# Kernel optimization log

Hardware: AMD Instinct MI355X
Metric: run time of the kernel (lower is better)

The kernel has to match this reference:

```python
import jax, jax.numpy as jnp
import numpy as np

H, D, DK, DV = 16, 1024, 64, 64
B, SQ, SK = 4, 1024, 1024
SCALE = float(np.power(D, 0.5))  # original scales by sqrt(num_dim), not sqrt(num_dim_k)


def setup_inputs() -> dict:
    key = jax.random.key(0)
    ks = jax.random.split(key, 8)
    xav_k = float(np.sqrt(2.0 / (D + DK)))
    xav_v = float(np.sqrt(2.0 / (D + DV)))
    return {
        "query": jax.random.normal(ks[0], (B, SQ, D), jnp.float32),
        "key": jax.random.normal(ks[1], (B, SK, D), jnp.float32),
        "value": jax.random.normal(ks[2], (B, SK, D), jnp.float32),
        "w_q": jax.random.normal(ks[3], (H, D, DK), jnp.float32) * xav_k,
        "w_k": jax.random.normal(ks[4], (H, D, DK), jnp.float32) * xav_k,
        "w_v": jax.random.normal(ks[5], (H, D, DV), jnp.float32) * xav_v,
        "w_proj": jax.random.normal(ks[6], (D, H * DV), jnp.float32) * float(np.sqrt(1.0 / (H * DV))),
        "b_proj": jnp.zeros((D,), jnp.float32),
    }


def reference(query, key, value, w_q, w_k, w_v, w_proj, b_proj):
    # per-head projections: [b,s,d] x [h,d,k] -> [b,h,s,k]
    q = jnp.einsum("bsd,hdk->bhsk", query, w_q)
    k = jnp.einsum("bsd,hdk->bhsk", key, w_k)
    v = jnp.einsum("bsd,hdv->bhsv", value, w_v)
    # scaled dot-product attention (dropout = identity in eval)
    scores = jnp.einsum("bhqk,bhsk->bhqs", q, k) / SCALE
    attn = jax.nn.softmax(scores, axis=-1)  # [b,h,sq,sk]
    out = jnp.einsum("bhqs,bhsv->bhqv", attn, v)
    # original: outs laid out [h*b, sq, dv], split by batch and cat on feature dim
    # -> heads concatenated along last dim: [b, sq, h*dv]
    out = out.transpose(0, 2, 1, 3).reshape(B, SQ, H * DV)
    out = out @ w_proj.T + b_proj  # Linear(H*DV -> D)
    # attns returned with head-major batch: [h*b, sq, sk]
    attns = attn.transpose(1, 0, 2, 3).reshape(H * B, SQ, SK)
    return (out, attns)
```

## Files before the change

### kernel.cpp

```cpp
#include <hip/hip_runtime.h>
#include <cstdint>

typedef __bf16 bf16;
typedef bf16 bf16x8 __attribute__((ext_vector_type(8)));
typedef bf16 bf16x4 __attribute__((ext_vector_type(4)));
typedef float f32x4 __attribute__((ext_vector_type(4)));

#define MFMA16(a, b, c) __builtin_amdgcn_mfma_f32_16x16x32_bf16((a), (b), (c), 0, 0, 0)

#define GLOBAL_TO_LDS16(gptr, lptr)                                          \
  __builtin_amdgcn_global_load_lds(                                          \
      (const __attribute__((address_space(1))) void*)(gptr),                 \
      (__attribute__((address_space(3))) void*)(lptr), 16, 0, 0)


__global__ __launch_bounds__(256) void cvt_all(
    const float* __restrict__ q, const float* __restrict__ k,
    const float* __restrict__ v, const float* __restrict__ wp,
    bf16* __restrict__ qb, bf16* __restrict__ kb,
    bf16* __restrict__ vb, bf16* __restrict__ wpb) {
  long i4 = ((long)blockIdx.x * 256 + threadIdx.x) * 4;
  const float* src;
  bf16* dst;
  long off;
  if (i4 < 4194304) {
    src = q; dst = qb; off = i4;
  } else if (i4 < 8388608) {
    src = k; dst = kb; off = i4 - 4194304;
  } else if (i4 < 12582912) {
    src = v; dst = vb; off = i4 - 8388608;
  } else {
    src = wp; dst = wpb; off = i4 - 12582912;
  }
  float4 f = *(const float4*)(src + off);
  bf16x4 o;
  o[0] = (bf16)f.x; o[1] = (bf16)f.y; o[2] = (bf16)f.z; o[3] = (bf16)f.w;
  *(bf16x4*)(dst + off) = o;
}

__global__ __launch_bounds__(256) void wtrans(
    const float* __restrict__ wq, const float* __restrict__ wk,
    const float* __restrict__ wv, bf16* __restrict__ wqT,
    bf16* __restrict__ wkT, bf16* __restrict__ wvT) {
  int z = blockIdx.z;
  const float* src = (z == 0) ? wq : ((z == 1) ? wk : wv);
  bf16* dst = (z == 0) ? wqT : ((z == 1) ? wkT : wvT);
  int t = blockIdx.x * 256 + threadIdx.x;
  int d = t & 1023;
  int r = t >> 10;
  int h = r >> 6, kk = r & 63;
  dst[t] = (bf16)src[(h << 16) + (d << 6) + kk];
}

__device__ __forceinline__ void gemm_mainloop(
    const bf16* __restrict__ A, const bf16* __restrict__ BT, bf16* As,
    bf16* Bs, int m0, int n0, f32x4 acc[4][4]) {
  const int tid = threadIdx.x;
  const int lane = tid & 63, wave = tid >> 6;
  const int wm = wave >> 1, wn = wave & 1;
  const int ln = lane & 15, ko8 = (lane >> 4) * 8;
  const int c0 = tid, c1 = 256 + tid;
  const int r0 = c0 >> 2, q0 = c0 & 3;
  const int r1 = c1 >> 2, q1 = c1 & 3;

  for (int k0 = 0; k0 < 1024; k0 += 32) {
    GLOBAL_TO_LDS16(A + (long)(m0 + r0) * 1024 + k0 + q0 * 8, As + c0 * 8);
    GLOBAL_TO_LDS16(A + (long)(m0 + r1) * 1024 + k0 + q1 * 8, As + c1 * 8);
    GLOBAL_TO_LDS16(BT + (long)(n0 + r0) * 1024 + k0 + q0 * 8, Bs + c0 * 8);
    GLOBAL_TO_LDS16(BT + (long)(n0 + r1) * 1024 + k0 + q1 * 8, Bs + c1 * 8);
    __syncthreads();
    bf16x8 af[4], bg[4];
#pragma unroll
    for (int t = 0; t < 4; ++t) {
      af[t] = *(const bf16x8*)(As + (wm * 64 + t * 16 + ln) * 32 + ko8);
      bg[t] = *(const bf16x8*)(Bs + (wn * 64 + t * 16 + ln) * 32 + ko8);
    }
#pragma unroll
    for (int i = 0; i < 4; ++i)
#pragma unroll
      for (int j = 0; j < 4; ++j) acc[i][j] = MFMA16(af[i], bg[j], acc[i][j]);
    __syncthreads();
  }
}

__global__ __launch_bounds__(256) void qkv_gemm(
    const bf16* __restrict__ qb, const bf16* __restrict__ kb,
    const bf16* __restrict__ vb, const bf16* __restrict__ wqT,
    const bf16* __restrict__ wkT, const bf16* __restrict__ wvT,
    bf16* __restrict__ Qd, bf16* __restrict__ Kd, bf16* __restrict__ Vtd) {
  __shared__ bf16 As[128 * 32];
  __shared__ bf16 Bs[128 * 32];
  int z = blockIdx.z;
  const bf16* A = (z == 0) ? qb : ((z == 1) ? kb : vb);
  const bf16* BT = (z == 0) ? wqT : ((z == 1) ? wkT : wvT);
  int m0 = blockIdx.x * 128, n0 = blockIdx.y * 128;
  f32x4 acc[4][4] = {};
  gemm_mainloop(A, BT, As, Bs, m0, n0, acc);

  const int tid = threadIdx.x, lane = tid & 63, wave = tid >> 6;
  const int wm = wave >> 1, wn = wave & 1, ln = lane & 15, lk = lane >> 4;
  const float alpha = (z == 0) ? 0.03125f : 1.0f;
  bf16* dstQK = (z == 0) ? Qd : Kd;
#pragma unroll
  for (int ti = 0; ti < 4; ++ti)
#pragma unroll
    for (int tj = 0; tj < 4; ++tj) {
      int n = n0 + wn * 64 + tj * 16 + ln;
#pragma unroll
      for (int i = 0; i < 4; ++i) {
        int m = m0 + wm * 64 + ti * 16 + lk * 4 + i;
        float vv = acc[ti][tj][i] * alpha;
        if (z <= 1) {
          long addr =
              ((((long)(m >> 10) * 16 + (n >> 6)) << 10) + (m & 1023)) * 64 +
              (n & 63);
          dstQK[addr] = (bf16)vv;
        } else {
          long addr =
              ((((long)(m >> 10) * 16 + (n >> 6)) << 6) + (n & 63)) * 1024 +
              (m & 1023);
          Vtd[addr] = (bf16)vv;
        }
      }
    }
}

__global__ __launch_bounds__(256) void attn_kernel(
    const bf16* __restrict__ Qd, const bf16* __restrict__ Kd,
    const bf16* __restrict__ Vtd, float* __restrict__ attns,
    bf16* __restrict__ Ob) {
  __shared__ bf16 P[16 * 1024];
  __shared__ float wstats[4][16][2];

  int qt = blockIdx.x, h = blockIdx.y, b = blockIdx.z;
  int q0 = qt * 16;
  int tid = threadIdx.x, lane = tid & 63, wave = tid >> 6;
  int ln = lane & 15, lk = lane >> 4;

  const bf16* Qbh = Qd + (((long)(b * 16 + h)) << 10) * 64;
  const bf16* Kbh = Kd + (((long)(b * 16 + h)) << 10) * 64;
  const bf16* Vbh = Vtd + (((long)(b * 16 + h)) << 6) * 1024;

  bf16x8 aq0 = *(const bf16x8*)(Qbh + (long)(q0 + ln) * 64 + lk * 8);
  bf16x8 aq1 = *(const bf16x8*)(Qbh + (long)(q0 + ln) * 64 + 32 + lk * 8);

  f32x4 sacc[16];
#pragma unroll
  for (int t = 0; t < 16; ++t) {
    int sk0 = wave * 256 + t * 16;
    f32x4 a = {0.f, 0.f, 0.f, 0.f};
    bf16x8 bk0 = *(const bf16x8*)(Kbh + (long)(sk0 + ln) * 64 + lk * 8);
    bf16x8 bk1 = *(const bf16x8*)(Kbh + (long)(sk0 + ln) * 64 + 32 + lk * 8);
    a = MFMA16(aq0, bk0, a);
    a = MFMA16(aq1, bk1, a);
    sacc[t] = a;
  }

  float mw[4], lw[4];
#pragma unroll
  for (int i = 0; i < 4; ++i) {
    float m = sacc[0][i];
#pragma unroll
    for (int t = 1; t < 16; ++t) m = fmaxf(m, sacc[t][i]);
#pragma unroll
    for (int off = 1; off < 16; off <<= 1) m = fmaxf(m, __shfl_xor(m, off, 64));
    mw[i] = m;
  }
#pragma unroll
  for (int i = 0; i < 4; ++i) {
    float s = 0.f;
#pragma unroll
    for (int t = 0; t < 16; ++t) {
      float e = __expf(sacc[t][i] - mw[i]);
      sacc[t][i] = e;
      s += e;
    }
#pragma unroll
    for (int off = 1; off < 16; off <<= 1) s += __shfl_xor(s, off, 64);
    lw[i] = s;
  }
  if (ln == 0) {
#pragma unroll
    for (int i = 0; i < 4; ++i) {
      wstats[wave][lk * 4 + i][0] = mw[i];
      wstats[wave][lk * 4 + i][1] = lw[i];
    }
  }
  __syncthreads();

  float fscale[4];
#pragma unroll
  for (int i = 0; i < 4; ++i) {
    int r = lk * 4 + i;
    float M = fmaxf(fmaxf(wstats[0][r][0], wstats[1][r][0]),
                    fmaxf(wstats[2][r][0], wstats[3][r][0]));
    float L = 0.f;
#pragma unroll
    for (int w = 0; w < 4; ++w)
      L += wstats[w][r][1] * __expf(wstats[w][r][0] - M);
    fscale[i] = __expf(mw[i] - M) / L;
  }

  float* arow_base = attns + ((((long)(h * 4 + b)) << 10) + q0) * 1024;
#pragma unroll
  for (int t = 0; t < 16; ++t) {
    int col = wave * 256 + t * 16 + ln;
    int g = col >> 3, cw = col & 7;
#pragma unroll
    for (int i = 0; i < 4; ++i) {
      int r = lk * 4 + i;
      float a = sacc[t][i] * fscale[i];
      arow_base[(long)r * 1024 + col] = a;
      P[(r << 10) + ((g ^ (r & 7)) << 3) + cw] = (bf16)a;
    }
  }
  __syncthreads();

  f32x4 oacc = {0.f, 0.f, 0.f, 0.f};
#pragma unroll 4
  for (int s0 = 0; s0 < 1024; s0 += 32) {
    int g = (s0 >> 3) + lk;
    bf16x8 ap = *(const bf16x8*)(P + (ln << 10) + ((g ^ (ln & 7)) << 3));
    bf16x8 bv =
        *(const bf16x8*)(Vbh + (long)(wave * 16 + ln) * 1024 + s0 + lk * 8);
    oacc = MFMA16(ap, bv, oacc);
  }
#pragma unroll
  for (int i = 0; i < 4; ++i) {
    int qrow = q0 + lk * 4 + i;
    Ob[((((long)b) << 10) + qrow) * 1024 + (h << 6) + wave * 16 + ln] =
        (bf16)oacc[i];
  }
}

__global__ __launch_bounds__(256) void out_gemm(
    const bf16* __restrict__ Ob, const bf16* __restrict__ wpb,
    const float* __restrict__ bias, float* __restrict__ out) {
  __shared__ bf16 As[128 * 32];
  __shared__ bf16 Bs[128 * 32];
  int m0 = blockIdx.x * 128, n0 = blockIdx.y * 128;
  f32x4 acc[4][4] = {};
  gemm_mainloop(Ob, wpb, As, Bs, m0, n0, acc);

  const int tid = threadIdx.x, lane = tid & 63, wave = tid >> 6;
  const int wm = wave >> 1, wn = wave & 1, ln = lane & 15, lk = lane >> 4;
#pragma unroll
  for (int ti = 0; ti < 4; ++ti)
#pragma unroll
    for (int tj = 0; tj < 4; ++tj) {
      int n = n0 + wn * 64 + tj * 16 + ln;
      float bn = bias[n];
#pragma unroll
      for (int i = 0; i < 4; ++i) {
        int m = m0 + wm * 64 + ti * 16 + lk * 4 + i;
        out[(long)m * 1024 + n] = acc[ti][tj][i] + bn;
      }
    }
}

extern "C" void kernel_launch(void* const* d_in, const int* in_sizes, int n_in,
                              void* d_out, int out_size, void* d_ws,
                              size_t ws_size, hipStream_t stream) {
  const float* query = (const float*)d_in[0];
  const float* key = (const float*)d_in[1];
  const float* value = (const float*)d_in[2];
  const float* w_q = (const float*)d_in[3];
  const float* w_k = (const float*)d_in[4];
  const float* w_v = (const float*)d_in[5];
  const float* w_proj = (const float*)d_in[6];
  const float* b_proj = (const float*)d_in[7];

  char* ws = (char*)d_ws;
  bf16* qb = (bf16*)(ws);
  bf16* kb = (bf16*)(ws + (8ul << 20));
  bf16* vb = (bf16*)(ws + (16ul << 20));
  bf16* wqT = (bf16*)(ws + (24ul << 20));
  bf16* wkT = (bf16*)(ws + (26ul << 20));
  bf16* wvT = (bf16*)(ws + (28ul << 20));
  bf16* wpb = (bf16*)(ws + (30ul << 20));
  bf16* Qd = (bf16*)(ws + (32ul << 20));
  bf16* Kd = (bf16*)(ws + (40ul << 20));
  bf16* Vtd = (bf16*)(ws + (48ul << 20));
  bf16* Ob = (bf16*)(ws + (56ul << 20));

  float* out = (float*)d_out;
  float* attns = out + 4194304;

  cvt_all<<<13312, 256, 0, stream>>>(query, key, value, w_proj, qb, kb, vb,
                                     wpb);
  wtrans<<<dim3(4096, 1, 3), 256, 0, stream>>>(w_q, w_k, w_v, wqT, wkT, wvT);
  qkv_gemm<<<dim3(32, 8, 3), 256, 0, stream>>>(qb, kb, vb, wqT, wkT, wvT, Qd,
                                               Kd, Vtd);
  attn_kernel<<<dim3(64, 16, 4), 256, 0, stream>>>(Qd, Kd, Vtd, attns, Ob);
  out_gemm<<<dim3(32, 8), 256, 0, stream>>>(Ob, wpb, b_proj, out);
}
```

Measured before the change: 521.8 us.

## Tile weight and V transposes through LDS and raise attention occupancy bound

Replaces the scalar strided weight transpose with an LDS-tiled transpose that reads float4 and writes 16-byte rows. The QKV GEMM now writes V in the same row-major layout as Q and K instead of a badly strided transposed scatter. A separate LDS-tiled kernel then transposes V for the attention kernel. The attention kernel also gains a min-2-blocks-per-CU launch bound. The cost is an extra kernel launch and an extra pass over V through memory, and the launch bound may cause register spills.

```diff
diff --git a/kernel.cpp b/kernel.cpp
--- a/kernel.cpp
+++ b/kernel.cpp
@@ -42,14 +42,51 @@
     const float* __restrict__ wq, const float* __restrict__ wk,
     const float* __restrict__ wv, bf16* __restrict__ wqT,
     bf16* __restrict__ wkT, bf16* __restrict__ wvT) {
-  int z = blockIdx.z;
-  const float* src = (z == 0) ? wq : ((z == 1) ? wk : wv);
-  bf16* dst = (z == 0) ? wqT : ((z == 1) ? wkT : wvT);
-  int t = blockIdx.x * 256 + threadIdx.x;
-  int d = t & 1023;
-  int r = t >> 10;
-  int h = r >> 6, kk = r & 63;
-  dst[t] = (bf16)src[(h << 16) + (d << 6) + kk];
+  __shared__ bf16 tile[64][72];
+  int dt = blockIdx.x, h = blockIdx.y, z = blockIdx.z;
+  const float* src =
+      ((z == 0) ? wq : (z == 1) ? wk : wv) + (long)h * 65536 + dt * 64 * 64;
+  bf16* dstM = (z == 0) ? wqT : (z == 1) ? wkT : wvT;
+  int t = threadIdx.x;
+#pragma unroll
+  for (int i = 0; i < 4; ++i) {
+    int chunk = t + i * 256;
+    int r = chunk >> 4, c4 = chunk & 15;
+    float4 f = *(const float4*)(src + r * 64 + c4 * 4);
+    bf16x4 o;
+    o[0] = (bf16)f.x; o[1] = (bf16)f.y; o[2] = (bf16)f.z; o[3] = (bf16)f.w;
+    *(bf16x4*)&tile[r][c4 * 4] = o;
+  }
+  __syncthreads();
+  int kk = t & 63, sc = t >> 6;
+  bf16 tmp[16];
+#pragma unroll
+  for (int j = 0; j < 16; ++j) tmp[j] = tile[sc * 16 + j][kk];
+  bf16* dst = dstM + ((long)h * 64 + kk) * 1024 + dt * 64 + sc * 16;
+  *(bf16x8*)dst = *(bf16x8*)tmp;
+  *(bf16x8*)(dst + 8) = *(bf16x8*)(tmp + 8);
+}
+
+__global__ __launch_bounds__(256) void vtrans(const bf16* __restrict__ Vd,
+                                              bf16* __restrict__ Vt) {
+  __shared__ bf16 tile[64][72];
+  int st = blockIdx.x, bh = blockIdx.y;
+  const bf16* src = Vd + ((long)bh * 1024 + st * 64) * 64;
+  int t = threadIdx.x;
+#pragma unroll
+  for (int i = 0; i < 2; ++i) {
+    int chunk = t + i * 256;
+    int r = chunk >> 3, c8 = chunk & 7;
+    *(bf16x8*)&tile[r][c8 * 8] = *(const bf16x8*)(src + r * 64 + c8 * 8);
+  }
+  __syncthreads();
+  int d = t & 63, sc = t >> 6;
+  bf16 tmp[16];
+#pragma unroll
+  for (int j = 0; j < 16; ++j) tmp[j] = tile[sc * 16 + j][d];
+  bf16* dst = Vt + ((long)bh * 64 + d) * 1024 + st * 64 + sc * 16;
+  *(bf16x8*)dst = *(bf16x8*)tmp;
+  *(bf16x8*)(dst + 8) = *(bf16x8*)(tmp + 8);
 }
 
 __device__ __forceinline__ void gemm_mainloop(
@@ -87,7 +124,7 @@
     const bf16* __restrict__ qb, const bf16* __restrict__ kb,
     const bf16* __restrict__ vb, const bf16* __restrict__ wqT,
     const bf16* __restrict__ wkT, const bf16* __restrict__ wvT,
-    bf16* __restrict__ Qd, bf16* __restrict__ Kd, bf16* __restrict__ Vtd) {
+    bf16* __restrict__ Qd, bf16* __restrict__ Kd, bf16* __restrict__ Vd) {
   __shared__ bf16 As[128 * 32];
   __shared__ bf16 Bs[128 * 32];
   int z = blockIdx.z;
@@ -100,7 +137,7 @@
   const int tid = threadIdx.x, lane = tid & 63, wave = tid >> 6;
   const int wm = wave >> 1, wn = wave & 1, ln = lane & 15, lk = lane >> 4;
   const float alpha = (z == 0) ? 0.03125f : 1.0f;
-  bf16* dstQK = (z == 0) ? Qd : Kd;
+  bf16* dst = (z == 0) ? Qd : ((z == 1) ? Kd : Vd);
 #pragma unroll
   for (int ti = 0; ti < 4; ++ti)
 #pragma unroll
@@ -109,23 +146,15 @@
 #pragma unroll
       for (int i = 0; i < 4; ++i) {
         int m = m0 + wm * 64 + ti * 16 + lk * 4 + i;
-        float vv = acc[ti][tj][i] * alpha;
-        if (z <= 1) {
-          long addr =
-              ((((long)(m >> 10) * 16 + (n >> 6)) << 10) + (m & 1023)) * 64 +
-              (n & 63);
-          dstQK[addr] = (bf16)vv;
-        } else {
-          long addr =
-              ((((long)(m >> 10) * 16 + (n >> 6)) << 6) + (n & 63)) * 1024 +
-              (m & 1023);
-          Vtd[addr] = (bf16)vv;
-        }
+        long addr =
+            ((((long)(m >> 10) * 16 + (n >> 6)) << 10) + (m & 1023)) * 64 +
+            (n & 63);
+        dst[addr] = (bf16)(acc[ti][tj][i] * alpha);
       }
     }
 }
 
-__global__ __launch_bounds__(256) void attn_kernel(
+__global__ __launch_bounds__(256, 2) void attn_kernel(
     const bf16* __restrict__ Qd, const bf16* __restrict__ Kd,
     const bf16* __restrict__ Vtd, float* __restrict__ attns,
     bf16* __restrict__ Ob) {
@@ -282,15 +311,17 @@
   bf16* Kd = (bf16*)(ws + (40ul << 20));
   bf16* Vtd = (bf16*)(ws + (48ul << 20));
   bf16* Ob = (bf16*)(ws + (56ul << 20));
+  bf16* Vd = (bf16*)(ws + (64ul << 20));
 
   float* out = (float*)d_out;
   float* attns = out + 4194304;
 
   cvt_all<<<13312, 256, 0, stream>>>(query, key, value, w_proj, qb, kb, vb,
                                      wpb);
-  wtrans<<<dim3(4096, 1, 3), 256, 0, stream>>>(w_q, w_k, w_v, wqT, wkT, wvT);
+  wtrans<<<dim3(16, 16, 3), 256, 0, stream>>>(w_q, w_k, w_v, wqT, wkT, wvT);
   qkv_gemm<<<dim3(32, 8, 3), 256, 0, stream>>>(qb, kb, vb, wqT, wkT, wvT, Qd,
-                                               Kd, Vtd);
+                                               Kd, Vd);
+  vtrans<<<dim3(16, 64), 256, 0, stream>>>(Vd, Vtd);
   attn_kernel<<<dim3(64, 16, 4), 256, 0, stream>>>(Qd, Kd, Vtd, attns, Ob);
   out_gemm<<<dim3(32, 8), 256, 0, stream>>>(Ob, wpb, b_proj, out);
 }
```

New measurement: 500.1 us. 4.2% less time.
